# Kernel tuning notes

Hardware: AMD Instinct MI355X
Metric: run time of the kernel (lower is better)

## Reference

```python
import jax, jax.numpy as jnp
import numpy as np
import math

B, N, D_MODEL, H = 4, 2048, 1024, 16
D_HEAD = D_MODEL // H

def setup_inputs() -> dict:
    key = jax.random.key(0)
    ks = jax.random.split(key, 9)
    s = 1.0 / math.sqrt(D_MODEL)
    inp = {
        "X_Q": jax.random.normal(ks[0], (B, N, D_MODEL), jnp.float32),
        "X_K": jax.random.normal(ks[1], (B, N, D_MODEL), jnp.float32),
        "X_V": jax.random.normal(ks[2], (B, N, D_MODEL), jnp.float32),
        # stacked per-head projection weights: [H, D_MODEL, D_HEAD] (y = x @ W + b)
        "Wq": jax.random.uniform(ks[3], (H, D_MODEL, D_HEAD), jnp.float32, -s, s),
        "Wk": jax.random.uniform(ks[4], (H, D_MODEL, D_HEAD), jnp.float32, -s, s),
        "Wv": jax.random.uniform(ks[5], (H, D_MODEL, D_HEAD), jnp.float32, -s, s),
        "bq": jax.random.uniform(ks[6], (H, D_HEAD), jnp.float32, -s, s),
        "bk": jax.random.uniform(ks[7], (H, D_HEAD), jnp.float32, -s, s),
        "bv": jax.random.uniform(ks[8], (H, D_HEAD), jnp.float32, -s, s),
    }
    return inp

def reference(X_Q, X_K, X_V, Wq, Wk, Wv, bq, bk, bv):
    # per-head projections, batched over heads: [B, H, N, D_HEAD]
    Q = jnp.einsum("bnd,hde->bhne", X_Q, Wq) + bq[None, :, None, :]
    K = jnp.einsum("bnd,hde->bhne", X_K, Wk) + bk[None, :, None, :]
    V = jnp.einsum("bnd,hde->bhne", X_V, Wv) + bv[None, :, None, :]
    scores = jnp.einsum("bhne,bhme->bhnm", Q, K)  # [B, H, N, N]
    # causal (att_mask=True): mask strictly-upper-triangular with -inf
    causal = jnp.tril(jnp.ones((N, N), dtype=bool))
    scores = jnp.where(causal[None, None], scores, -jnp.inf)
    # original divides AFTER masking; -inf stays -inf so equivalent
    probs = jax.nn.softmax(scores / math.sqrt(D_HEAD), axis=-1)
    out = jnp.einsum("bhnm,bhme->bhne", probs, V)  # [B, H, N, D_HEAD]
    # concat heads along feature dim
    return out.transpose(0, 2, 1, 3).reshape(B, N, D_MODEL)
```

## Files before the change

### kernel.cpp

```cpp
#include <hip/hip_runtime.h>

typedef _Float16 half8  __attribute__((ext_vector_type(8)));
typedef _Float16 half4v __attribute__((ext_vector_type(4)));
typedef _Float16 half2v __attribute__((ext_vector_type(2)));
typedef float    floatx4 __attribute__((ext_vector_type(4)));

#define B_   4
#define N_   2048
#define DM_  1024
#define H_   16
#define DH_  64

static const size_t XEL = (size_t)B_ * N_ * DM_;
static const size_t WEL = (size_t)DM_ * DM_;
static const size_t QEL = (size_t)B_ * H_ * N_ * DH_;

#define GLOAD_LDS16(src, dst) \
  __builtin_amdgcn_global_load_lds((const __attribute__((address_space(1))) void*)(src), \
                                   (__attribute__((address_space(3))) void*)(dst), 16, 0, 0)

__global__ void cvt_x(const float* __restrict__ x0, const float* __restrict__ x1,
                      const float* __restrict__ x2, _Float16* __restrict__ out) {
  const int z = blockIdx.z;
  const float* x = (z == 0) ? x0 : (z == 1 ? x1 : x2);
  _Float16* o = out + (size_t)z * XEL;
  const size_t i = ((size_t)blockIdx.x * 256 + threadIdx.x) * 4;
  float4 v = *(const float4*)(x + i);
  half4v h;
  h[0] = (_Float16)v.x; h[1] = (_Float16)v.y; h[2] = (_Float16)v.z; h[3] = (_Float16)v.w;
  *(half4v*)(o + i) = h;
}

__global__ void cvt_w(const float* __restrict__ w0, const float* __restrict__ w1,
                      const float* __restrict__ w2, _Float16* __restrict__ out) {
  const int z = blockIdx.z;
  const float* w = (z == 0) ? w0 : (z == 1 ? w1 : w2);
  _Float16* o = out + (size_t)z * WEL;
  const int idx = blockIdx.x * 256 + threadIdx.x;
  const int n = idx >> 10, k = idx & 1023;
  const int h = n >> 6, e = n & 63;
  o[idx] = (_Float16)w[((size_t)h * 1024 + k) * 64 + e];
}

__global__ __launch_bounds__(256, 4) void qkv_gemm(const _Float16* __restrict__ X16,
                                                   const _Float16* __restrict__ W16t,
                                                   const float* __restrict__ b0,
                                                   const float* __restrict__ b1,
                                                   const float* __restrict__ b2,
                                                   _Float16* __restrict__ QKV) {
  __shared__ char smem[32768];
  const int lid = blockIdx.x;
  const int win = lid >> 6;
  const int i6  = lid & 63;
  const int n0i = i6 >> 3;
  const int c   = i6 & 7;
  const int g   = win * 8 + c;
  const int z   = g >> 6;
  const int row0 = (g & 63) * 128;
  const int n0   = n0i * 128;

  const _Float16* X = X16 + (size_t)z * XEL;
  const _Float16* W = W16t + (size_t)z * WEL;
  const float* bias = (z == 0) ? b0 : (z == 1 ? b1 : b2);
  const float osc = (z == 0) ? 0.18033688011112042f : 1.0f;
  _Float16* out = QKV + (size_t)z * QEL;

  const int tid = threadIdx.x;
  const int w   = tid >> 6;
  const int l   = tid & 63;
  const int lg  = l >> 4, lr = l & 15;
  const int wm  = w >> 1, wn = w & 1;

  floatx4 zf = {0.f, 0.f, 0.f, 0.f};
  floatx4 acc[4][4];
#pragma unroll
  for (int mi = 0; mi < 4; ++mi)
#pragma unroll
    for (int ni = 0; ni < 4; ++ni) acc[mi][ni] = zf;

  auto STAGE = [&](int kt, int bufc) {
    char* Ab = smem + bufc * 16384;
    char* Bb = Ab + 8192;
    const int k0 = kt * 32;
#pragma unroll
    for (int i = 0; i < 2; ++i) {
      const int q   = i * 4 + w;
      const int row = q * 16 + (l >> 2);
      const int kb  = (l & 3) ^ ((row >> 1) & 3);
      GLOAD_LDS16(X + (size_t)(row0 + row) * 1024 + k0 + kb * 8, Ab + q * 1024);
      GLOAD_LDS16(W + (size_t)(n0  + row) * 1024 + k0 + kb * 8, Bb + q * 1024);
    }
  };

  STAGE(0, 0);
  __syncthreads();

  for (int kt = 0; kt < 32; ++kt) {
    const int cur = kt & 1;
    if (kt + 1 < 32) STAGE(kt + 1, cur ^ 1);
    char* Al = smem + cur * 16384;
    char* Bl = Al + 8192;

    half8 af[4], bf[4];
#pragma unroll
    for (int mi = 0; mi < 4; ++mi) {
      const int row = wm * 64 + mi * 16 + lr;
      const int ch  = lg ^ ((row >> 1) & 3);
      af[mi] = *(const half8*)(Al + row * 64 + ch * 16);
    }
#pragma unroll
    for (int ni = 0; ni < 4; ++ni) {
      const int col = wn * 64 + ni * 16 + lr;
      const int ch  = lg ^ ((col >> 1) & 3);
      bf[ni] = *(const half8*)(Bl + col * 64 + ch * 16);
    }
#pragma unroll
    for (int mi = 0; mi < 4; ++mi)
#pragma unroll
      for (int ni = 0; ni < 4; ++ni)
        acc[mi][ni] = __builtin_amdgcn_mfma_f32_16x16x32_f16(af[mi], bf[ni], acc[mi][ni], 0, 0, 0);

    __syncthreads();
  }

#pragma unroll
  for (int mi = 0; mi < 4; ++mi)
#pragma unroll
    for (int ni = 0; ni < 4; ++ni) {
      const int gc = n0 + wn * 64 + ni * 16 + lr;
      const float bv = bias[gc];
      const int h = gc >> 6, e = gc & 63;
#pragma unroll
      for (int j = 0; j < 4; ++j) {
        const int gr = row0 + wm * 64 + mi * 16 + lg * 4 + j;
        const int b = gr >> 11, n = gr & 2047;
        out[(((size_t)(b * 16 + h)) * 2048 + n) * 64 + e] = (_Float16)((acc[mi][ni][j] + bv) * osc);
      }
    }
}

__global__ void vtrans(const _Float16* __restrict__ V16, _Float16* __restrict__ Vt) {
  __shared__ _Float16 t[64 * 72];
  const int bh = blockIdx.y;
  const int n0 = blockIdx.x * 64;
  const int tid = threadIdx.x;
#pragma unroll
  for (int it = 0; it < 2; ++it) {
    const int L = it * 256 + tid;
    const int n = L >> 3, cb = L & 7;
    half8 v = *(const half8*)(V16 + ((size_t)bh * 2048 + n0 + n) * 64 + cb * 8);
    *(half8*)(t + n * 72 + cb * 8) = v;
  }
  __syncthreads();
#pragma unroll
  for (int it = 0; it < 2; ++it) {
    const int L = it * 256 + tid;
    const int d = L >> 3, cb = L & 7;
    half8 v;
#pragma unroll
    for (int u = 0; u < 8; ++u) v[u] = t[(cb * 8 + u) * 72 + d];
    *(half8*)(Vt + ((size_t)bh * 64 + d) * 2048 + n0 + cb * 8) = v;
  }
}

__global__ __launch_bounds__(512, 4) void attn(const _Float16* __restrict__ Q16,
                                               const _Float16* __restrict__ K16,
                                               const _Float16* __restrict__ Vt16,
                                               float* __restrict__ out) {
  __shared__ char smem[49152];
  const int lid = blockIdx.x;
  const int bh = (lid & 7) | ((lid >> 6) << 3);
  const int bx = (lid >> 3) & 7;
  const int tid = threadIdx.x;
  const int w = tid >> 6, l = tid & 63;
  const int lg = l >> 4, lr = l & 15;
  const int b = bh >> 4, h = bh & 15;

  char* Pl = smem + 32768 + w * 2048;
  int cur = 0;

  auto STAGE = [&](int t, int bufc) {
    const int c0t = t * 64;
    char* Kb = smem + bufc * 16384;
    char* Vb = Kb + 8192;
    const int row = w * 8 + (l >> 3);
    const int kb = l & 7;
    const int ks = (kb ^ (row & 7)) << 3;
    GLOAD_LDS16(K16 + ((size_t)bh * 2048 + c0t + row) * 64 + ks, Kb + w * 1024);
    GLOAD_LDS16(Vt16 + ((size_t)bh * 64 + row) * 2048 + c0t + ks, Vb + w * 1024);
  };

  for (int ph = 0; ph < 2; ++ph) {
    const int qt = ph ? (15 - bx) : bx;
    const int q0 = qt * 128;
    const int wr0 = q0 + w * 16;
    const int nt = 2 * (qt + 1);

    half8 qf[2];
#pragma unroll
    for (int kk = 0; kk < 2; ++kk)
      qf[kk] = *(const half8*)(Q16 + ((size_t)bh * 2048 + wr0 + lr) * 64 + kk * 32 + lg * 8);

    floatx4 zf = {0.f, 0.f, 0.f, 0.f};
    floatx4 O[4];
#pragma unroll
    for (int dt = 0; dt < 4; ++dt) O[dt] = zf;
    float mrow = -3.0e38f;
    float lden = 0.f;

    STAGE(0, cur);
    __syncthreads();

    for (int t = 0; t < nt; ++t) {
      if (t + 1 < nt) STAGE(t + 1, cur ^ 1);
      const int c0 = t * 64;
      char* Kl = smem + cur * 16384;
      char* Vl = Kl + 8192;

      if (c0 <= wr0 + 15) {
        floatx4 s[4];
#pragma unroll
        for (int cb = 0; cb < 4; ++cb) s[cb] = zf;
#pragma unroll
        for (int kk = 0; kk < 2; ++kk)
#pragma unroll
          for (int cb = 0; cb < 4; ++cb) {
            const int cc = cb * 16 + lr;
            const int ch = (kk * 4 + lg) ^ (cc & 7);
            half8 kf = *(const half8*)(Kl + cc * 128 + ch * 16);
            s[cb] = __builtin_amdgcn_mfma_f32_16x16x32_f16(kf, qf[kk], s[cb], 0, 0, 0);
          }

        float tm = -3.0e38f;
        if (c0 + 63 > wr0) {
          const int r = wr0 + lr;
#pragma unroll
          for (int cb = 0; cb < 4; ++cb)
#pragma unroll
            for (int j = 0; j < 4; ++j) {
              const int cc = c0 + cb * 16 + lg * 4 + j;
              float x = s[cb][j];
              x = (cc > r) ? -3.0e38f : x;
              s[cb][j] = x;
              tm = fmaxf(tm, x);
            }
        } else {
#pragma unroll
          for (int cb = 0; cb < 4; ++cb)
#pragma unroll
            for (int j = 0; j < 4; ++j) tm = fmaxf(tm, s[cb][j]);
        }
        tm = fmaxf(tm, __shfl_xor(tm, 16, 64));
        tm = fmaxf(tm, __shfl_xor(tm, 32, 64));

        float scl = 1.0f;
        if (__any(tm > mrow + 8.0f)) {
          const float mn = fmaxf(mrow, tm);
          scl = __builtin_amdgcn_exp2f(mrow - mn);
          mrow = mn;
          const float s0 = __shfl(scl, lg * 4 + 0, 64);
          const float s1 = __shfl(scl, lg * 4 + 1, 64);
          const float s2 = __shfl(scl, lg * 4 + 2, 64);
          const float s3 = __shfl(scl, lg * 4 + 3, 64);
#pragma unroll
          for (int dt = 0; dt < 4; ++dt) {
            O[dt][0] *= s0; O[dt][1] *= s1; O[dt][2] *= s2; O[dt][3] *= s3;
          }
        }

        float tsum = 0.f;
#pragma unroll
        for (int cb = 0; cb < 4; ++cb)
#pragma unroll
          for (int j = 0; j < 4; ++j) {
            const float p = __builtin_amdgcn_exp2f(s[cb][j] - mrow);
            s[cb][j] = p;
            tsum += p;
          }
        tsum += __shfl_xor(tsum, 16, 64);
        tsum += __shfl_xor(tsum, 32, 64);
        lden = lden * scl + tsum;

#pragma unroll
        for (int cb = 0; cb < 4; ++cb) {
          const int cbase = cb * 16 + lg * 4;
          half4v hv;
          hv[0] = (_Float16)s[cb][0]; hv[1] = (_Float16)s[cb][1];
          hv[2] = (_Float16)s[cb][2]; hv[3] = (_Float16)s[cb][3];
          *(half4v*)(Pl + lr * 128 + (((cbase >> 3) ^ (lr & 7)) << 4) + ((cbase & 7) << 1)) = hv;
        }
        asm volatile("s_waitcnt lgkmcnt(0)" ::: "memory");
        __builtin_amdgcn_sched_barrier(0);

#pragma unroll
        for (int kc = 0; kc < 2; ++kc) {
          const int chp = (kc * 4 + lg) ^ (lr & 7);
          half8 pa = *(const half8*)(Pl + lr * 128 + chp * 16);
#pragma unroll
          for (int dt = 0; dt < 4; ++dt) {
            const int d = dt * 16 + lr;
            const int ch = (kc * 4 + lg) ^ (d & 7);
            half8 vb = *(const half8*)(Vl + d * 128 + ch * 16);
            O[dt] = __builtin_amdgcn_mfma_f32_16x16x32_f16(pa, vb, O[dt], 0, 0, 0);
          }
        }
      }

      __syncthreads();
      cur ^= 1;
    }

    float inv[4];
#pragma unroll
    for (int j = 0; j < 4; ++j) {
      const float lj = __shfl(lden, lg * 4 + j, 64);
      inv[j] = 1.0f / lj;
    }
#pragma unroll
    for (int dt = 0; dt < 4; ++dt)
#pragma unroll
      for (int j = 0; j < 4; ++j) {
        const int n = wr0 + lg * 4 + j;
        out[((size_t)(b * 2048 + n)) * 1024 + h * 64 + dt * 16 + lr] = O[dt][j] * inv[j];
      }
  }
}

extern "C" void kernel_launch(void* const* d_in, const int* in_sizes, int n_in,
                              void* d_out, int out_size, void* d_ws, size_t ws_size,
                              hipStream_t stream) {
  const float* XQ = (const float*)d_in[0];
  const float* XK = (const float*)d_in[1];
  const float* XV = (const float*)d_in[2];
  const float* Wq = (const float*)d_in[3];
  const float* Wk = (const float*)d_in[4];
  const float* Wv = (const float*)d_in[5];
  const float* bq = (const float*)d_in[6];
  const float* bk = (const float*)d_in[7];
  const float* bv = (const float*)d_in[8];

  char* ws = (char*)d_ws;
  _Float16* X16  = (_Float16*)(ws + 0);
  _Float16* W16t = (_Float16*)(ws + 50331648);
  _Float16* QKV  = (_Float16*)(ws + 56623104);
  _Float16* Vt   = (_Float16*)(ws + 106954752);

  cvt_x<<<dim3(8192, 1, 3), 256, 0, stream>>>(XQ, XK, XV, X16);
  cvt_w<<<dim3(4096, 1, 3), 256, 0, stream>>>(Wq, Wk, Wv, W16t);
  qkv_gemm<<<dim3(1536), 256, 0, stream>>>(X16, W16t, bq, bk, bv, QKV);
  vtrans<<<dim3(32, 64), 256, 0, stream>>>(QKV + 2 * QEL, Vt);
  attn<<<dim3(512), 512, 0, stream>>>(QKV, QKV + QEL, Vt, (float*)d_out);
}
```

Before: 173.5 us.

## Deepen QKV GEMM K-tile to 64 with explicit vmcnt-based async pipelining

Doubles the K tile of the QKV projection GEMM from 32 to 64, so the staged LDS buffers grow to 64 KB and the number of K iterations halves. A 3-bit XOR swizzle over 128-byte rows replaces the old 2-bit swizzle. Each iteration now waits with an explicit s_waitcnt vmcnt(8) for only the current stage's loads before a raw s_barrier, so the next stage's global-to-LDS copies keep running during compute, and sched_barriers pin the instruction order. The aim is fewer barriers per K and better load/compute overlap. In exchange, occupancy drops from 4 to 2 blocks per CU, and the hand-written waitcnt counts depend on exactly 8 outstanding loads per stage.

```diff
diff --git a/kernel.cpp b/kernel.cpp
--- a/kernel.cpp
+++ b/kernel.cpp
@@ -42,13 +42,13 @@
   o[idx] = (_Float16)w[((size_t)h * 1024 + k) * 64 + e];
 }
 
-__global__ __launch_bounds__(256, 4) void qkv_gemm(const _Float16* __restrict__ X16,
+__global__ __launch_bounds__(256, 2) void qkv_gemm(const _Float16* __restrict__ X16,
                                                    const _Float16* __restrict__ W16t,
                                                    const float* __restrict__ b0,
                                                    const float* __restrict__ b1,
                                                    const float* __restrict__ b2,
                                                    _Float16* __restrict__ QKV) {
-  __shared__ char smem[32768];
+  __shared__ char smem[65536];
   const int lid = blockIdx.x;
   const int win = lid >> 6;
   const int i6  = lid & 63;
@@ -79,48 +79,57 @@
     for (int ni = 0; ni < 4; ++ni) acc[mi][ni] = zf;
 
   auto STAGE = [&](int kt, int bufc) {
-    char* Ab = smem + bufc * 16384;
-    char* Bb = Ab + 8192;
-    const int k0 = kt * 32;
-#pragma unroll
-    for (int i = 0; i < 2; ++i) {
-      const int q   = i * 4 + w;
-      const int row = q * 16 + (l >> 2);
-      const int kb  = (l & 3) ^ ((row >> 1) & 3);
-      GLOAD_LDS16(X + (size_t)(row0 + row) * 1024 + k0 + kb * 8, Ab + q * 1024);
-      GLOAD_LDS16(W + (size_t)(n0  + row) * 1024 + k0 + kb * 8, Bb + q * 1024);
+    char* Ab = smem + bufc * 32768;
+    char* Bb = Ab + 16384;
+    const int k0 = kt * 64;
+#pragma unroll
+    for (int it = 0; it < 4; ++it) {
+      const int C   = (it * 4 + w) * 64 + l;
+      const int row = C >> 3, kb = C & 7;
+      const int ks  = (kb ^ (row & 7)) << 3;
+      GLOAD_LDS16(X + (size_t)(row0 + row) * 1024 + k0 + ks, Ab + (it * 4 + w) * 1024);
+      GLOAD_LDS16(W + (size_t)(n0  + row) * 1024 + k0 + ks, Bb + (it * 4 + w) * 1024);
     }
   };
 
   STAGE(0, 0);
-  __syncthreads();
-
-  for (int kt = 0; kt < 32; ++kt) {
+
+  for (int kt = 0; kt < 16; ++kt) {
     const int cur = kt & 1;
-    if (kt + 1 < 32) STAGE(kt + 1, cur ^ 1);
-    char* Al = smem + cur * 16384;
-    char* Bl = Al + 8192;
-
-    half8 af[4], bf[4];
-#pragma unroll
-    for (int mi = 0; mi < 4; ++mi) {
-      const int row = wm * 64 + mi * 16 + lr;
-      const int ch  = lg ^ ((row >> 1) & 3);
-      af[mi] = *(const half8*)(Al + row * 64 + ch * 16);
-    }
-#pragma unroll
-    for (int ni = 0; ni < 4; ++ni) {
-      const int col = wn * 64 + ni * 16 + lr;
-      const int ch  = lg ^ ((col >> 1) & 3);
-      bf[ni] = *(const half8*)(Bl + col * 64 + ch * 16);
-    }
-#pragma unroll
-    for (int mi = 0; mi < 4; ++mi)
-#pragma unroll
-      for (int ni = 0; ni < 4; ++ni)
-        acc[mi][ni] = __builtin_amdgcn_mfma_f32_16x16x32_f16(af[mi], bf[ni], acc[mi][ni], 0, 0, 0);
-
-    __syncthreads();
+    if (kt + 1 < 16) {
+      STAGE(kt + 1, cur ^ 1);
+      asm volatile("s_waitcnt vmcnt(8)" ::: "memory");
+    } else {
+      asm volatile("s_waitcnt vmcnt(0)" ::: "memory");
+    }
+    __builtin_amdgcn_s_barrier();
+    __builtin_amdgcn_sched_barrier(0);
+
+    char* Al = smem + cur * 32768;
+    char* Bl = Al + 16384;
+#pragma unroll
+    for (int kk = 0; kk < 2; ++kk) {
+      half8 af[4], bf[4];
+#pragma unroll
+      for (int mi = 0; mi < 4; ++mi) {
+        const int row = wm * 64 + mi * 16 + lr;
+        const int ch  = (kk * 4 + lg) ^ (row & 7);
+        af[mi] = *(const half8*)(Al + row * 128 + ch * 16);
+      }
+#pragma unroll
+      for (int ni = 0; ni < 4; ++ni) {
+        const int col = wn * 64 + ni * 16 + lr;
+        const int ch  = (kk * 4 + lg) ^ (col & 7);
+        bf[ni] = *(const half8*)(Bl + col * 128 + ch * 16);
+      }
+#pragma unroll
+      for (int mi = 0; mi < 4; ++mi)
+#pragma unroll
+        for (int ni = 0; ni < 4; ++ni)
+          acc[mi][ni] = __builtin_amdgcn_mfma_f32_16x16x32_f16(af[mi], bf[ni], acc[mi][ni], 0, 0, 0);
+    }
+    __builtin_amdgcn_sched_barrier(0);
+    __builtin_amdgcn_s_barrier();
   }
 
 #pragma unroll
```

Measured after the change: 167.0 us. -3.8%, faster.

## Triple-buffer QKV GEMM, use explicit vmcnt waits, precompute LDS addresses in attention

Applied to the files above, without the earlier changes.

The QKV projection GEMM moves from double to triple buffering in LDS (48KB, occupancy hint lowered to 3) and prefetches two k-tiles ahead. It replaces __syncthreads with explicit vmcnt waits plus raw s_barrier, so global-to-LDS loads can stay in flight across iterations. The attention kernel gets the same partial vmcnt wait and barrier scheme, and its swizzled LDS addresses for K, V and P are hoisted out of the loop into per-lane offsets. The aim is to hide load latency and cut address arithmetic, at the cost of more LDS and fewer resident blocks for the GEMM.

```diff
diff --git a/kernel.cpp b/kernel.cpp
--- a/kernel.cpp
+++ b/kernel.cpp
@@ -42,13 +42,13 @@
   o[idx] = (_Float16)w[((size_t)h * 1024 + k) * 64 + e];
 }
 
-__global__ __launch_bounds__(256, 4) void qkv_gemm(const _Float16* __restrict__ X16,
+__global__ __launch_bounds__(256, 3) void qkv_gemm(const _Float16* __restrict__ X16,
                                                    const _Float16* __restrict__ W16t,
                                                    const float* __restrict__ b0,
                                                    const float* __restrict__ b1,
                                                    const float* __restrict__ b2,
                                                    _Float16* __restrict__ QKV) {
-  __shared__ char smem[32768];
+  __shared__ char smem[49152];
   const int lid = blockIdx.x;
   const int win = lid >> 6;
   const int i6  = lid & 63;
@@ -92,35 +92,43 @@
     }
   };
 
+  const int chq = (lg ^ ((lr >> 1) & 3)) * 16;
+  const int aA  = wm * 4096 + lr * 64 + chq;
+  const int aB  = wn * 4096 + lr * 64 + chq;
+
   STAGE(0, 0);
-  __syncthreads();
+  STAGE(1, 1);
+  int rb = 0, wb = 2;
 
   for (int kt = 0; kt < 32; ++kt) {
-    const int cur = kt & 1;
-    if (kt + 1 < 32) STAGE(kt + 1, cur ^ 1);
-    char* Al = smem + cur * 16384;
-    char* Bl = Al + 8192;
-
+    if (kt + 2 < 32) {
+      STAGE(kt + 2, wb);
+      wb = (wb == 2) ? 0 : wb + 1;
+      asm volatile("s_waitcnt vmcnt(8)" ::: "memory");
+    } else if (kt == 30) {
+      asm volatile("s_waitcnt vmcnt(4)" ::: "memory");
+    } else {
+      asm volatile("s_waitcnt vmcnt(0)" ::: "memory");
+    }
+    __builtin_amdgcn_s_barrier();
+    __builtin_amdgcn_sched_barrier(0);
+
+    const char* Al = smem + rb * 16384;
+    const char* Bl = Al + 8192;
     half8 af[4], bf[4];
 #pragma unroll
-    for (int mi = 0; mi < 4; ++mi) {
-      const int row = wm * 64 + mi * 16 + lr;
-      const int ch  = lg ^ ((row >> 1) & 3);
-      af[mi] = *(const half8*)(Al + row * 64 + ch * 16);
-    }
-#pragma unroll
-    for (int ni = 0; ni < 4; ++ni) {
-      const int col = wn * 64 + ni * 16 + lr;
-      const int ch  = lg ^ ((col >> 1) & 3);
-      bf[ni] = *(const half8*)(Bl + col * 64 + ch * 16);
-    }
+    for (int mi = 0; mi < 4; ++mi) af[mi] = *(const half8*)(Al + aA + mi * 1024);
+#pragma unroll
+    for (int ni = 0; ni < 4; ++ni) bf[ni] = *(const half8*)(Bl + aB + ni * 1024);
 #pragma unroll
     for (int mi = 0; mi < 4; ++mi)
 #pragma unroll
       for (int ni = 0; ni < 4; ++ni)
         acc[mi][ni] = __builtin_amdgcn_mfma_f32_16x16x32_f16(af[mi], bf[ni], acc[mi][ni], 0, 0, 0);
 
-    __syncthreads();
+    __builtin_amdgcn_sched_barrier(0);
+    __builtin_amdgcn_s_barrier();
+    rb = (rb == 2) ? 0 : rb + 1;
   }
 
 #pragma unroll
@@ -176,7 +184,17 @@
   const int lg = l >> 4, lr = l & 15;
   const int b = bh >> 4, h = bh & 15;
 
-  char* Pl = smem + 32768 + w * 2048;
+  const int sz = lr & 7;
+  const int aK0 = lr * 128 + ((lg ^ sz) * 16);
+  const int aK1 = lr * 128 + (((4 + lg) ^ sz) * 16);
+  const int pbase = 32768 + w * 2048 + lr * 128;
+  int aPw[4];
+#pragma unroll
+  for (int cb = 0; cb < 4; ++cb)
+    aPw[cb] = pbase + (((2 * cb + (lg >> 1)) ^ sz) << 4) + ((lg & 1) * 8);
+  const int aPr0 = pbase + ((lg ^ sz) << 4);
+  const int aPr1 = pbase + (((4 + lg) ^ sz) << 4);
+
   int cur = 0;
 
   auto STAGE = [&](int t, int bufc) {
@@ -209,27 +227,34 @@
     float lden = 0.f;
 
     STAGE(0, cur);
-    __syncthreads();
 
     for (int t = 0; t < nt; ++t) {
-      if (t + 1 < nt) STAGE(t + 1, cur ^ 1);
+      if (t + 1 < nt) {
+        STAGE(t + 1, cur ^ 1);
+        asm volatile("s_waitcnt vmcnt(2)" ::: "memory");
+      } else {
+        asm volatile("s_waitcnt vmcnt(0)" ::: "memory");
+      }
+      __builtin_amdgcn_s_barrier();
+      __builtin_amdgcn_sched_barrier(0);
+
       const int c0 = t * 64;
-      char* Kl = smem + cur * 16384;
-      char* Vl = Kl + 8192;
+      const char* Kb = smem + cur * 16384;
 
       if (c0 <= wr0 + 15) {
         floatx4 s[4];
 #pragma unroll
         for (int cb = 0; cb < 4; ++cb) s[cb] = zf;
 #pragma unroll
-        for (int kk = 0; kk < 2; ++kk)
-#pragma unroll
-          for (int cb = 0; cb < 4; ++cb) {
-            const int cc = cb * 16 + lr;
-            const int ch = (kk * 4 + lg) ^ (cc & 7);
-            half8 kf = *(const half8*)(Kl + cc * 128 + ch * 16);
-            s[cb] = __builtin_amdgcn_mfma_f32_16x16x32_f16(kf, qf[kk], s[cb], 0, 0, 0);
-          }
+        for (int cb = 0; cb < 4; ++cb) {
+          half8 kf = *(const half8*)(Kb + aK0 + cb * 2048);
+          s[cb] = __builtin_amdgcn_mfma_f32_16x16x32_f16(kf, qf[0], s[cb], 0, 0, 0);
+        }
+#pragma unroll
+        for (int cb = 0; cb < 4; ++cb) {
+          half8 kf = *(const half8*)(Kb + aK1 + cb * 2048);
+          s[cb] = __builtin_amdgcn_mfma_f32_16x16x32_f16(kf, qf[1], s[cb], 0, 0, 0);
+        }
 
         float tm = -3.0e38f;
         if (c0 + 63 > wr0) {
@@ -246,9 +271,11 @@
             }
         } else {
 #pragma unroll
-          for (int cb = 0; cb < 4; ++cb)
-#pragma unroll
-            for (int j = 0; j < 4; ++j) tm = fmaxf(tm, s[cb][j]);
+          for (int cb = 0; cb < 4; ++cb) {
+            const float m01 = fmaxf(s[cb][0], s[cb][1]);
+            const float m23 = fmaxf(s[cb][2], s[cb][3]);
+            tm = fmaxf(tm, fmaxf(m01, m23));
+          }
         }
         tm = fmaxf(tm, __shfl_xor(tm, 16, 64));
         tm = fmaxf(tm, __shfl_xor(tm, 32, 64));
@@ -283,30 +310,32 @@
 
 #pragma unroll
         for (int cb = 0; cb < 4; ++cb) {
-          const int cbase = cb * 16 + lg * 4;
           half4v hv;
           hv[0] = (_Float16)s[cb][0]; hv[1] = (_Float16)s[cb][1];
           hv[2] = (_Float16)s[cb][2]; hv[3] = (_Float16)s[cb][3];
-          *(half4v*)(Pl + lr * 128 + (((cbase >> 3) ^ (lr & 7)) << 4) + ((cbase & 7) << 1)) = hv;
+          *(half4v*)(smem + aPw[cb]) = hv;
         }
         asm volatile("s_waitcnt lgkmcnt(0)" ::: "memory");
         __builtin_amdgcn_sched_barrier(0);
 
-#pragma unroll
-        for (int kc = 0; kc < 2; ++kc) {
-          const int chp = (kc * 4 + lg) ^ (lr & 7);
-          half8 pa = *(const half8*)(Pl + lr * 128 + chp * 16);
+        {
+          half8 pa = *(const half8*)(smem + aPr0);
 #pragma unroll
           for (int dt = 0; dt < 4; ++dt) {
-            const int d = dt * 16 + lr;
-            const int ch = (kc * 4 + lg) ^ (d & 7);
-            half8 vb = *(const half8*)(Vl + d * 128 + ch * 16);
+            half8 vb = *(const half8*)(Kb + 8192 + aK0 + dt * 2048);
             O[dt] = __builtin_amdgcn_mfma_f32_16x16x32_f16(pa, vb, O[dt], 0, 0, 0);
           }
+          pa = *(const half8*)(smem + aPr1);
+#pragma unroll
+          for (int dt = 0; dt < 4; ++dt) {
+            half8 vb = *(const half8*)(Kb + 8192 + aK1 + dt * 2048);
+            O[dt] = __builtin_amdgcn_mfma_f32_16x16x32_f16(pa, vb, O[dt], 0, 0, 0);
+          }
         }
       }
 
-      __syncthreads();
+      __builtin_amdgcn_sched_barrier(0);
+      __builtin_amdgcn_s_barrier();
       cur ^= 1;
     }
 
```

Result: no change. 173.6 us (+0.0%).
